# Optimization experiments

Hardware: AMD Instinct MI355X
Metric: run time of the kernel (lower is better)

Reference implementation:

```python
import jax, jax.numpy as jnp
import numpy as np

_EPS = 1e-8
_WENO_EPS = 1e-6
_BETA = 0.01
_MIN_RATIO = 0.3
_MAX_RATIO = 5.0


def _weno3_reconstruct(v_mm, v_m, v_p):
    d0, d1 = 1.0 / 3.0, 2.0 / 3.0
    # left-biased (u_minus)
    beta0_m = jnp.square(v_mm - v_m)
    beta1_m = jnp.square(v_m - v_p)
    alpha0_m = d0 / jnp.square(_WENO_EPS + beta0_m)
    alpha1_m = d1 / jnp.square(_WENO_EPS + beta1_m)
    w0_m = alpha0_m / (alpha0_m + alpha1_m)
    u_minus = w0_m * (0.5 * (-v_mm + 3.0 * v_m)) + (1.0 - w0_m) * (0.5 * (v_m + v_p))
    # right-biased (u_plus)
    beta0_p = jnp.square(v_p - v_m)
    beta1_p = jnp.square(v_m - v_mm)
    alpha0_p = d0 / jnp.square(_WENO_EPS + beta0_p)
    alpha1_p = d1 / jnp.square(_WENO_EPS + beta1_p)
    w0_p = alpha0_p / (alpha0_p + alpha1_p)
    u_plus = w0_p * (0.5 * (-v_p + 3.0 * v_m)) + (1.0 - w0_p) * (0.5 * (v_m + v_mm))
    return u_minus, u_plus


def _weno3_gradient(field):
    u = jnp.pad(field, ((0, 0), (0, 0), (2, 2), (2, 2)), mode='edge')
    # x-direction forward differences at offsets
    vx_mm = u[..., 2:-2, 1:-3] - u[..., 2:-2, 0:-4]
    vx_m = u[..., 2:-2, 2:-2] - u[..., 2:-2, 1:-3]
    vx_c = u[..., 2:-2, 3:-1] - u[..., 2:-2, 2:-2]
    vx_p = u[..., 2:-2, 4:] - u[..., 2:-2, 3:-1]
    ux_minus, _ = _weno3_reconstruct(vx_mm, vx_m, vx_c)
    _, ux_plus = _weno3_reconstruct(vx_m, vx_c, vx_p)
    grad_x = jnp.maximum(jax.nn.relu(ux_minus), jax.nn.relu(-ux_plus))
    # y-direction
    vy_mm = u[..., 1:-3, 2:-2] - u[..., 0:-4, 2:-2]
    vy_m = u[..., 2:-2, 2:-2] - u[..., 1:-3, 2:-2]
    vy_c = u[..., 3:-1, 2:-2] - u[..., 2:-2, 2:-2]
    vy_p = u[..., 4:, 2:-2] - u[..., 3:-1, 2:-2]
    uy_minus, _ = _weno3_reconstruct(vy_mm, vy_m, vy_c)
    _, uy_plus = _weno3_reconstruct(vy_m, vy_c, vy_p)
    grad_y = jnp.maximum(jax.nn.relu(uy_minus), jax.nn.relu(-uy_plus))
    return grad_x, grad_y


def setup_inputs() -> dict:
    key = jax.random.key(0)
    k1, k2 = jax.random.split(key)
    pred_dist = jax.random.normal(k1, (32, 1, 512, 512), dtype=jnp.float32)
    reachable = jax.random.uniform(k2, (32, 1, 512, 512), dtype=jnp.float32)
    return {"pred_dist": pred_dist, "reachable": reachable}


def reference(pred_dist, reachable):
    gx, gy = _weno3_gradient(pred_dist)
    gmag = jnp.sqrt(jnp.square(gx) + jnp.square(gy) + _EPS)
    H, W = pred_dist.shape[-2:]
    h, w = max(H - 1, 1), max(W - 1, 1)
    target = 1.0 / float(np.sqrt(h * h + w * w))
    residual = gmag - target
    abs_r = jnp.abs(residual)
    # smooth L1 (beta=0.01)
    per_pixel = jnp.where(abs_r < _BETA, 0.5 * jnp.square(residual) / _BETA, abs_r - 0.5 * _BETA)
    mask = (reachable > 0.5).astype(per_pixel.dtype)
    valid = ((gmag >= _MIN_RATIO * target) & (gmag <= _MAX_RATIO * target)).astype(per_pixel.dtype)
    final_mask = mask * valid
    num = jnp.sum(per_pixel * final_mask)
    den = jnp.maximum(jnp.sum(final_mask), _EPS)
    return num / den
```

## Files before the change

### kernel.cpp

```cpp
#include <hip/hip_runtime.h>

#define B_  32
#define H_  512
#define W_  512
#define HW_ (H_ * W_)
#define NWAVE_ 8192
#define TPB_  64

typedef float f32x4 __attribute__((ext_vector_type(4)));

__device__ __forceinline__ float rcp_fast(float x) { return __builtin_amdgcn_rcpf(x); }

__device__ __forceinline__ f32x4 rcp4(f32x4 v) {
    f32x4 r;
    r.x = rcp_fast(v.x); r.y = rcp_fast(v.y);
    r.z = rcp_fast(v.z); r.w = rcp_fast(v.w);
    return r;
}

__device__ __forceinline__ f32x4 sq4(f32x4 sd) {
    f32x4 t = sd * sd + 1e-6f;
    return t * t;
}

__device__ __forceinline__ float core(float sOut, float sMid,
                                      float fMain, float fOut, float fPair) {
    float p0 = 1.5f * fMain - 0.5f * fOut;
    float p1 = 0.5f * (fMain + fPair);
    float s2 = sOut + sOut;
    return (sMid * p0 + s2 * p1) * rcp_fast(sMid + s2);
}

__device__ __forceinline__ f32x4 coreV(f32x4 sOut, f32x4 sMid,
                                       f32x4 fMain, f32x4 fOut, f32x4 fPair) {
    f32x4 p0 = 1.5f * fMain - 0.5f * fOut;
    f32x4 p1 = 0.5f * (fMain + fPair);
    f32x4 s2 = sOut + sOut;
    return (sMid * p0 + s2 * p1) * rcp4(sMid + s2);
}

__device__ __forceinline__ f32x4 gyV(f32x4 um, f32x4 up) {
    f32x4 g;
    g.x = fmaxf(fmaxf(um.x, -up.x), 0.0f);
    g.y = fmaxf(fmaxf(um.y, -up.y), 0.0f);
    g.z = fmaxf(fmaxf(um.z, -up.z), 0.0f);
    g.w = fmaxf(fmaxf(um.w, -up.w), 0.0f);
    return g;
}

__device__ __forceinline__ void row_process(
        f32x4 c0, f32x4 c1,
        f32x4 gy0, f32x4 gy1,
        f32x4 q0, f32x4 q1,
        int lane, float target, float lo, float hi,
        float& num, float& den) {
    float xm2 = __shfl_up(c1.z, 1);
    float xm1 = __shfl_up(c1.w, 1);
    float xp1 = __shfl_down(c0.x, 1);
    float xp2 = __shfl_down(c0.y, 1);
    if (lane == 0)  { xm2 = c0.x; xm1 = c0.x; }
    if (lane == 63) { xp1 = c1.w; xp2 = c1.w; }

    float D[11];
    D[0]  = xm1  - xm2;
    D[1]  = c0.x - xm1;
    D[2]  = c0.y - c0.x;
    D[3]  = c0.z - c0.y;
    D[4]  = c0.w - c0.z;
    D[5]  = c1.x - c0.w;
    D[6]  = c1.y - c1.x;
    D[7]  = c1.z - c1.y;
    D[8]  = c1.w - c1.z;
    D[9]  = xp1  - c1.w;
    D[10] = xp2  - xp1;

    float s[10];
    #pragma unroll
    for (int k = 0; k < 10; ++k) {
        float sd = D[k] - D[k + 1];
        float t = fmaf(sd, sd, 1e-6f);
        s[k] = t * t;
    }

    #pragma unroll
    for (int i = 0; i < 8; ++i) {
        float um = core(s[i],     s[i + 1], D[i + 1], D[i],     D[i + 2]);
        float up = core(s[i + 2], s[i + 1], D[i + 2], D[i + 3], D[i + 1]);
        float gx = fmaxf(fmaxf(um, -up), 0.0f);
        float gy = (i < 4) ? gy0[i] : gy1[i - 4];
        float q  = (i < 4) ? q0[i]  : q1[i - 4];

        float gmag = __builtin_amdgcn_sqrtf(fmaf(gx, gx, fmaf(gy, gy, 1e-8f)));
        float r  = gmag - target;
        float ar = fabsf(r);
        float pp = (ar < 0.01f) ? (50.0f * r * r) : (ar - 0.005f);
        bool  m  = (q > 0.5f) && (gmag >= lo) && (gmag <= hi);
        float sel = m ? 1.0f : 0.0f;
        num = fmaf(sel, pp, num);
        den += sel;
    }
}

__device__ __forceinline__ int clampy(int v) {
    return v < 0 ? 0 : (v > H_ - 1 ? H_ - 1 : v);
}

__global__ __launch_bounds__(TPB_) void eikonal_main(
        const float* __restrict__ pred, const float* __restrict__ reach,
        float2* __restrict__ partials) {
    const float target = 1.0f / sqrtf((float)(511 * 511 + 511 * 511));
    const float lo = 0.3f * target;
    const float hi = 5.0f * target;

    int lane = threadIdx.x & 63;

    int wv = ((blockIdx.x & 7) << 10) + (blockIdx.x >> 3);
    int b  = wv >> 8;
    int y0 = (wv & 255) << 1;

    const float* brow = pred + b * HW_;
    int x0 = lane << 3;

    const float* rA = brow + (clampy(y0 - 2) << 9) + x0;
    const float* rB = brow + (clampy(y0 - 1) << 9) + x0;
    const float* rC = brow + ((y0    ) << 9) + x0;
    const float* rD = brow + ((y0 + 1) << 9) + x0;
    const float* rE = brow + (clampy(y0 + 2) << 9) + x0;
    const float* rF = brow + (clampy(y0 + 3) << 9) + x0;
    const float* qCp = reach + b * HW_ + ((y0    ) << 9) + x0;
    const float* qDp = reach + b * HW_ + ((y0 + 1) << 9) + x0;

    f32x4 pA0 = *(const f32x4*)(rA);     f32x4 pA1 = *(const f32x4*)(rA + 4);
    f32x4 pB0 = *(const f32x4*)(rB);     f32x4 pB1 = *(const f32x4*)(rB + 4);
    f32x4 pC0 = *(const f32x4*)(rC);     f32x4 pC1 = *(const f32x4*)(rC + 4);
    f32x4 pD0 = *(const f32x4*)(rD);     f32x4 pD1 = *(const f32x4*)(rD + 4);
    f32x4 pE0 = *(const f32x4*)(rE);     f32x4 pE1 = *(const f32x4*)(rE + 4);
    f32x4 pF0 = *(const f32x4*)(rF);     f32x4 pF1 = *(const f32x4*)(rF + 4);
    f32x4 qC0 = *(const f32x4*)(qCp);    f32x4 qC1 = *(const f32x4*)(qCp + 4);
    f32x4 qD0 = *(const f32x4*)(qDp);    f32x4 qD1 = *(const f32x4*)(qDp + 4);

    asm volatile("" ::
        "v"(pA0), "v"(pA1), "v"(pB0), "v"(pB1),
        "v"(pC0), "v"(pC1), "v"(pD0), "v"(pD1),
        "v"(pE0), "v"(pE1), "v"(pF0), "v"(pF1),
        "v"(qC0), "v"(qC1), "v"(qD0), "v"(qD1));
    __builtin_amdgcn_sched_barrier(0);

    f32x4 dBA0 = pB0 - pA0, dBA1 = pB1 - pA1;
    f32x4 dCB0 = pC0 - pB0, dCB1 = pC1 - pB1;
    f32x4 dDC0 = pD0 - pC0, dDC1 = pD1 - pC1;
    f32x4 dED0 = pE0 - pD0, dED1 = pE1 - pD1;
    f32x4 dFE0 = pF0 - pE0, dFE1 = pF1 - pE1;

    f32x4 sy0_0 = sq4(dBA0 - dCB0), sy0_1 = sq4(dBA1 - dCB1);
    f32x4 sy1_0 = sq4(dCB0 - dDC0), sy1_1 = sq4(dCB1 - dDC1);
    f32x4 sy2_0 = sq4(dDC0 - dED0), sy2_1 = sq4(dDC1 - dED1);
    f32x4 sy3_0 = sq4(dED0 - dFE0), sy3_1 = sq4(dED1 - dFE1);

    f32x4 gyC0 = gyV(coreV(sy0_0, sy1_0, dCB0, dBA0, dDC0),
                     coreV(sy2_0, sy1_0, dDC0, dED0, dCB0));
    f32x4 gyC1 = gyV(coreV(sy0_1, sy1_1, dCB1, dBA1, dDC1),
                     coreV(sy2_1, sy1_1, dDC1, dED1, dCB1));
    f32x4 gyD0 = gyV(coreV(sy1_0, sy2_0, dDC0, dCB0, dED0),
                     coreV(sy3_0, sy2_0, dED0, dFE0, dDC0));
    f32x4 gyD1 = gyV(coreV(sy1_1, sy2_1, dDC1, dCB1, dED1),
                     coreV(sy3_1, sy2_1, dED1, dFE1, dDC1));

    float num = 0.0f, den = 0.0f;

    row_process(pC0, pC1, gyC0, gyC1, qC0, qC1, lane, target, lo, hi, num, den);
    row_process(pD0, pD1, gyD0, gyD1, qD0, qD1, lane, target, lo, hi, num, den);

    #pragma unroll
    for (int off = 32; off > 0; off >>= 1) {
        num += __shfl_xor(num, off);
        den += __shfl_xor(den, off);
    }
    if (lane == 0) {
        partials[wv] = make_float2(num, den);
    }
}

__global__ __launch_bounds__(512) void eikonal_finalize(
        const float2* __restrict__ partials, float* __restrict__ out) {
    int t = threadIdx.x;
    double n = 0.0, d = 0.0;
    #pragma unroll
    for (int k = 0; k < NWAVE_ / 512; ++k) {
        float2 p = partials[t + (k << 9)];
        n += (double)p.x;
        d += (double)p.y;
    }
    #pragma unroll
    for (int off = 32; off > 0; off >>= 1) {
        n += __shfl_down(n, off);
        d += __shfl_down(d, off);
    }
    __shared__ double sn[8], sd[8];
    int wid = t >> 6;
    int lane = t & 63;
    if (lane == 0) { sn[wid] = n; sd[wid] = d; }
    __syncthreads();
    if (t == 0) {
        double fn = 0.0, fd = 0.0;
        #pragma unroll
        for (int k = 0; k < 8; ++k) { fn += sn[k]; fd += sd[k]; }
        if (fd < 1e-8) fd = 1e-8;
        out[0] = (float)(fn / fd);
    }
}

extern "C" void kernel_launch(void* const* d_in, const int* in_sizes, int n_in,
                              void* d_out, int out_size, void* d_ws, size_t ws_size,
                              hipStream_t stream) {
    const float* pred  = (const float*)d_in[0];
    const float* reach = (const float*)d_in[1];
    float* out = (float*)d_out;
    float2* partials = (float2*)d_ws;

    eikonal_main<<<NWAVE_, TPB_, 0, stream>>>(pred, reach, partials);
    eikonal_finalize<<<1, 512, 0, stream>>>(partials, out);
}
```

Measured before the change: 26.92 us.

## Pack two waves per block, stream reachable mask nontemporally, simplify WENO core

Launches 4096 blocks of 128 threads, two waves per block, instead of 8192 single-wave blocks, and keeps the XCD-aware block swizzle with the wave index made uniform. The reachable-mask loads become nontemporal, since that data is read only once and should not pollute the cache. The WENO weight core is rewritten algebraically as w*diff + 0.5*a using FMAs, which trims a few ALU operations per reconstruction. This changes floating-point rounding slightly and alters how blocks are scheduled.

```diff
diff --git a/kernel.cpp b/kernel.cpp
--- a/kernel.cpp
+++ b/kernel.cpp
@@ -5,7 +5,8 @@
 #define W_  512
 #define HW_ (H_ * W_)
 #define NWAVE_ 8192
-#define TPB_  64
+#define NBLK_ 4096
+#define TPB_  128
 
 typedef float f32x4 __attribute__((ext_vector_type(4)));
 
@@ -25,18 +26,22 @@
 
 __device__ __forceinline__ float core(float sOut, float sMid,
                                       float fMain, float fOut, float fPair) {
-    float p0 = 1.5f * fMain - 0.5f * fOut;
-    float p1 = 0.5f * (fMain + fPair);
-    float s2 = sOut + sOut;
-    return (sMid * p0 + s2 * p1) * rcp_fast(sMid + s2);
+    float a    = fMain + fPair;
+    float b    = fOut + fPair;
+    float diff = fmaf(-0.5f, b, fMain);
+    float den  = fmaf(2.0f, sOut, sMid);
+    float w    = sMid * rcp_fast(den);
+    return fmaf(w, diff, 0.5f * a);
 }
 
 __device__ __forceinline__ f32x4 coreV(f32x4 sOut, f32x4 sMid,
                                        f32x4 fMain, f32x4 fOut, f32x4 fPair) {
-    f32x4 p0 = 1.5f * fMain - 0.5f * fOut;
-    f32x4 p1 = 0.5f * (fMain + fPair);
-    f32x4 s2 = sOut + sOut;
-    return (sMid * p0 + s2 * p1) * rcp4(sMid + s2);
+    f32x4 a    = fMain + fPair;
+    f32x4 b    = fOut + fPair;
+    f32x4 diff = fMain - 0.5f * b;
+    f32x4 den  = sMid + 2.0f * sOut;
+    f32x4 w    = sMid * rcp4(den);
+    return w * diff + 0.5f * a;
 }
 
 __device__ __forceinline__ f32x4 gyV(f32x4 um, f32x4 up) {
@@ -112,9 +117,11 @@
     const float lo = 0.3f * target;
     const float hi = 5.0f * target;
 
-    int lane = threadIdx.x & 63;
-
-    int wv = ((blockIdx.x & 7) << 10) + (blockIdx.x >> 3);
+    int t = threadIdx.x;
+    int lane = t & 63;
+
+    int bswz = ((blockIdx.x & 7) << 9) + (blockIdx.x >> 3);
+    int wv = __builtin_amdgcn_readfirstlane((bswz << 1) + (t >> 6));
     int b  = wv >> 8;
     int y0 = (wv & 255) << 1;
 
@@ -127,8 +134,8 @@
     const float* rD = brow + ((y0 + 1) << 9) + x0;
     const float* rE = brow + (clampy(y0 + 2) << 9) + x0;
     const float* rF = brow + (clampy(y0 + 3) << 9) + x0;
-    const float* qCp = reach + b * HW_ + ((y0    ) << 9) + x0;
-    const float* qDp = reach + b * HW_ + ((y0 + 1) << 9) + x0;
+    const f32x4* qCp = (const f32x4*)(reach + b * HW_ + ((y0    ) << 9) + x0);
+    const f32x4* qDp = (const f32x4*)(reach + b * HW_ + ((y0 + 1) << 9) + x0);
 
     f32x4 pA0 = *(const f32x4*)(rA);     f32x4 pA1 = *(const f32x4*)(rA + 4);
     f32x4 pB0 = *(const f32x4*)(rB);     f32x4 pB1 = *(const f32x4*)(rB + 4);
@@ -136,8 +143,10 @@
     f32x4 pD0 = *(const f32x4*)(rD);     f32x4 pD1 = *(const f32x4*)(rD + 4);
     f32x4 pE0 = *(const f32x4*)(rE);     f32x4 pE1 = *(const f32x4*)(rE + 4);
     f32x4 pF0 = *(const f32x4*)(rF);     f32x4 pF1 = *(const f32x4*)(rF + 4);
-    f32x4 qC0 = *(const f32x4*)(qCp);    f32x4 qC1 = *(const f32x4*)(qCp + 4);
-    f32x4 qD0 = *(const f32x4*)(qDp);    f32x4 qD1 = *(const f32x4*)(qDp + 4);
+    f32x4 qC0 = __builtin_nontemporal_load(qCp);
+    f32x4 qC1 = __builtin_nontemporal_load(qCp + 1);
+    f32x4 qD0 = __builtin_nontemporal_load(qDp);
+    f32x4 qD1 = __builtin_nontemporal_load(qDp + 1);
 
     asm volatile("" ::
         "v"(pA0), "v"(pA1), "v"(pB0), "v"(pB1),
@@ -218,6 +227,6 @@
     float* out = (float*)d_out;
     float2* partials = (float2*)d_ws;
 
-    eikonal_main<<<NWAVE_, TPB_, 0, stream>>>(pred, reach, partials);
+    eikonal_main<<<NBLK_, TPB_, 0, stream>>>(pred, reach, partials);
     eikonal_finalize<<<1, 512, 0, stream>>>(partials, out);
 }
```

After: 25.01 us. 7.1% less time.
